# Optimization experiments

Measured on AMD Instinct MI355X. Metric: run time of the kernel, lower is better.

The kernel has to match this reference:

```python
import jax, jax.numpy as jnp
import numpy as np

K = 3  # kernel_size; padding = 1, stride = 1


def setup_inputs() -> dict:
    key = jax.random.key(0)
    ks = jax.random.split(key, 3)
    b, c, h, w = 8, 96, 256, 256
    x = jax.random.normal(ks[0], (b, c, h, w), dtype=jnp.float32)
    # attention MLP params: 1x1 convs on pooled vector == dense layers
    w1 = jax.random.normal(ks[1], (c // 8, c), dtype=jnp.float32) * (1.0 / np.sqrt(c))
    b1 = jnp.zeros((c // 8,), dtype=jnp.float32)
    w2 = jax.random.normal(ks[2], (K * K, c // 8), dtype=jnp.float32) * (1.0 / np.sqrt(c // 8))
    b2 = jnp.zeros((K * K,), dtype=jnp.float32)
    return {"x": x, "w1": w1, "b1": b1, "w2": w2, "b2": b2}


def reference(x, w1, b1, w2, b2):
    b, c, h, w = x.shape
    # attention: global avg pool -> 1x1 conv -> relu -> 1x1 conv -> softmax over k^2
    pooled = x.mean(axis=(2, 3))                       # (b, c)
    hid = jax.nn.relu(pooled @ w1.T + b1)              # (b, c//8)
    kw = jax.nn.softmax(hid @ w2.T + b2, axis=1)       # (b, k^2), per-batch kernel
    # dynamic depthwise conv: weighted sum of k^2 shifted views (no unfold materialization)
    xp = jnp.pad(x, ((0, 0), (0, 0), (1, 1), (1, 1)))
    out = jnp.zeros_like(x)
    for p in range(K * K):  # F.unfold ordering: row-major over kernel window
        di, dj = p // K, p % K
        out = out + kw[:, p, None, None, None] * xp[:, :, di:di + h, dj:dj + w]
    return out
```

## Files before the change

kernel.cpp:

```cpp
#include <hip/hip_runtime.h>
#include <math.h>


#define NB 8
#define NC 96
#define HH 256
#define WW 256
#define PLANE (HH * WW)
#define NPLANES (NB * NC)

__global__ __launch_bounds__(256) void pool_kernel(const float* __restrict__ x,
                                                   float* __restrict__ pooled) {
    const int plane = blockIdx.x;
    const int tid = threadIdx.x;
    const float4* xp = (const float4*)x + (size_t)plane * (PLANE / 4);
    float s = 0.f;
#pragma unroll 8
    for (int k = 0; k < 64; ++k) {
        float4 v = xp[k * 256 + tid];
        s += v.x + v.y + v.z + v.w;
    }
#pragma unroll
    for (int off = 32; off > 0; off >>= 1) s += __shfl_down(s, off);
    __shared__ float ws[4];
    if ((tid & 63) == 0) ws[tid >> 6] = s;
    __syncthreads();
    if (tid == 0)
        pooled[plane] = (ws[0] + ws[1] + ws[2] + ws[3]) * (1.0f / (float)PLANE);
}

__global__ __launch_bounds__(128) void attn_kernel(const float* __restrict__ pooled,
                                                   const float* __restrict__ w1,
                                                   const float* __restrict__ b1,
                                                   const float* __restrict__ w2,
                                                   const float* __restrict__ b2,
                                                   float* __restrict__ kw) {
    const int b = blockIdx.x;
    const int tid = threadIdx.x;
    __shared__ float p[NC];
    __shared__ float hid[12];
    __shared__ float logit[9];
    if (tid < NC) p[tid] = pooled[b * NC + tid];
    __syncthreads();
    if (tid < 12) {
        float a = b1[tid];
#pragma unroll
        for (int c = 0; c < NC; ++c) a = fmaf(p[c], w1[tid * NC + c], a);
        hid[tid] = a > 0.f ? a : 0.f;
    }
    __syncthreads();
    if (tid < 9) {
        float a = b2[tid];
#pragma unroll
        for (int j = 0; j < 12; ++j) a = fmaf(hid[j], w2[tid * 12 + j], a);
        logit[tid] = a;
    }
    __syncthreads();
    if (tid == 0) {
        float m = logit[0];
#pragma unroll
        for (int q = 1; q < 9; ++q) m = fmaxf(m, logit[q]);
        float e[9], s = 0.f;
#pragma unroll
        for (int q = 0; q < 9; ++q) { e[q] = __expf(logit[q] - m); s += e[q]; }
        float inv = 1.f / s;
#pragma unroll
        for (int q = 0; q < 9; ++q) kw[b * 9 + q] = e[q] * inv;
    }
}

__device__ __forceinline__ void accum_row(const float* __restrict__ row, int t,
                                          float w0, float w1, float w2, float4& o) {
    const int jc = t << 2;
    float4 cc = *(const float4*)(row + jc);
    float lm = (t > 0) ? row[jc - 1] : 0.f;
    float rp = (t < (WW / 4 - 1)) ? row[jc + 4] : 0.f;
    o.x = fmaf(w0, lm,   fmaf(w1, cc.x, fmaf(w2, cc.y, o.x)));
    o.y = fmaf(w0, cc.x, fmaf(w1, cc.y, fmaf(w2, cc.z, o.y)));
    o.z = fmaf(w0, cc.y, fmaf(w1, cc.z, fmaf(w2, cc.w, o.z)));
    o.w = fmaf(w0, cc.z, fmaf(w1, cc.w, fmaf(w2, rp,   o.w)));
}

__global__ __launch_bounds__(256) void conv_kernel(const float* __restrict__ x,
                                                   const float* __restrict__ kw9,
                                                   float* __restrict__ out) {
    const int q = blockIdx.x * 256 + threadIdx.x;
    const int i = q >> 6;
    const int t = q & 63;

    const size_t base = ((size_t)(blockIdx.z * NC + blockIdx.y)) * PLANE;
    const float* xpl = x + base;

    float w[9];
#pragma unroll
    for (int p = 0; p < 9; ++p) w[p] = kw9[blockIdx.z * 9 + p];

    float4 o = {0.f, 0.f, 0.f, 0.f};
    if (i > 0)        accum_row(xpl + (size_t)(i - 1) * WW, t, w[0], w[1], w[2], o);
                      accum_row(xpl + (size_t)i * WW,       t, w[3], w[4], w[5], o);
    if (i < HH - 1)   accum_row(xpl + (size_t)(i + 1) * WW, t, w[6], w[7], w[8], o);

    *(float4*)(out + base + (size_t)i * WW + (t << 2)) = o;
}

extern "C" void kernel_launch(void* const* d_in, const int* in_sizes, int n_in,
                              void* d_out, int out_size, void* d_ws, size_t ws_size,
                              hipStream_t stream) {
    const float* x  = (const float*)d_in[0];
    const float* w1 = (const float*)d_in[1];
    const float* b1 = (const float*)d_in[2];
    const float* w2 = (const float*)d_in[3];
    const float* b2 = (const float*)d_in[4];
    float* out = (float*)d_out;

    float* pooled = (float*)d_ws;
    float* kw     = pooled + NPLANES;

    pool_kernel<<<NPLANES, 256, 0, stream>>>(x, pooled);
    attn_kernel<<<NB, 128, 0, stream>>>(pooled, w1, b1, w2, b2, kw);
    dim3 grid(PLANE / (4 * 256), NC, NB);
    conv_kernel<<<grid, 256, 0, stream>>>(x, kw, out);
}
```

Before: 424.9 us.

## Stream rows per wavefront with register reuse, shuffled halos, and nontemporal stores

The conv kernel now gives each 64-lane wavefront a strip of 32 rows and slides a three-row register window down it. Each input row is loaded once instead of three times. Horizontal halo values come from wavefront shuffles instead of extra scalar global loads, and outputs use nontemporal stores. The grid shrinks to 2x96x8 blocks (1536 blocks of 256 threads, 6144 wavefronts), so there is less parallelism and a serial dependency along rows, which may limit latency hiding.

```diff
diff --git a/kernel.cpp b/kernel.cpp
--- a/kernel.cpp
+++ b/kernel.cpp
@@ -9,15 +9,17 @@
 #define PLANE (HH * WW)
 #define NPLANES (NB * NC)
 
+typedef float vfloat4 __attribute__((ext_vector_type(4)));
+
 __global__ __launch_bounds__(256) void pool_kernel(const float* __restrict__ x,
                                                    float* __restrict__ pooled) {
     const int plane = blockIdx.x;
     const int tid = threadIdx.x;
-    const float4* xp = (const float4*)x + (size_t)plane * (PLANE / 4);
+    const vfloat4* xp = (const vfloat4*)x + (size_t)plane * (PLANE / 4);
     float s = 0.f;
 #pragma unroll 8
     for (int k = 0; k < 64; ++k) {
-        float4 v = xp[k * 256 + tid];
+        vfloat4 v = xp[k * 256 + tid];
         s += v.x + v.y + v.z + v.w;
     }
 #pragma unroll
@@ -69,38 +71,62 @@
     }
 }
 
-__device__ __forceinline__ void accum_row(const float* __restrict__ row, int t,
-                                          float w0, float w1, float w2, float4& o) {
-    const int jc = t << 2;
-    float4 cc = *(const float4*)(row + jc);
-    float lm = (t > 0) ? row[jc - 1] : 0.f;
-    float rp = (t < (WW / 4 - 1)) ? row[jc + 4] : 0.f;
-    o.x = fmaf(w0, lm,   fmaf(w1, cc.x, fmaf(w2, cc.y, o.x)));
-    o.y = fmaf(w0, cc.x, fmaf(w1, cc.y, fmaf(w2, cc.z, o.y)));
-    o.z = fmaf(w0, cc.y, fmaf(w1, cc.z, fmaf(w2, cc.w, o.z)));
-    o.w = fmaf(w0, cc.z, fmaf(w1, cc.w, fmaf(w2, rp,   o.w)));
+struct Row {
+    vfloat4 v;
+    float hl, hr;
+};
+
+__device__ __forceinline__ Row load_row(const float* __restrict__ rowp, int lane) {
+    Row r;
+    r.v = *(const vfloat4*)(rowp + (lane << 2));
+    float up = __shfl_up(r.v.w, 1);
+    float dn = __shfl_down(r.v.x, 1);
+    r.hl = (lane == 0) ? 0.f : up;
+    r.hr = (lane == 63) ? 0.f : dn;
+    return r;
+}
+
+__device__ __forceinline__ Row zero_row() {
+    Row r; r.v = (vfloat4){0.f, 0.f, 0.f, 0.f}; r.hl = 0.f; r.hr = 0.f; return r;
+}
+
+__device__ __forceinline__ void row_fma(const Row& r, float wl, float wc, float wr,
+                                        vfloat4& o) {
+    o.x = fmaf(wl, r.hl,  fmaf(wc, r.v.x, fmaf(wr, r.v.y, o.x)));
+    o.y = fmaf(wl, r.v.x, fmaf(wc, r.v.y, fmaf(wr, r.v.z, o.y)));
+    o.z = fmaf(wl, r.v.y, fmaf(wc, r.v.z, fmaf(wr, r.v.w, o.z)));
+    o.w = fmaf(wl, r.v.z, fmaf(wc, r.v.w, fmaf(wr, r.hr,  o.w)));
 }
 
 __global__ __launch_bounds__(256) void conv_kernel(const float* __restrict__ x,
                                                    const float* __restrict__ kw9,
                                                    float* __restrict__ out) {
-    const int q = blockIdx.x * 256 + threadIdx.x;
-    const int i = q >> 6;
-    const int t = q & 63;
+    const int lane = threadIdx.x & 63;
+    const int strip = (blockIdx.x << 2) + (threadIdx.x >> 6);
+    const int rs = strip << 5;
 
     const size_t base = ((size_t)(blockIdx.z * NC + blockIdx.y)) * PLANE;
     const float* xpl = x + base;
+    float* opl = out + base;
 
     float w[9];
 #pragma unroll
     for (int p = 0; p < 9; ++p) w[p] = kw9[blockIdx.z * 9 + p];
 
-    float4 o = {0.f, 0.f, 0.f, 0.f};
-    if (i > 0)        accum_row(xpl + (size_t)(i - 1) * WW, t, w[0], w[1], w[2], o);
-                      accum_row(xpl + (size_t)i * WW,       t, w[3], w[4], w[5], o);
-    if (i < HH - 1)   accum_row(xpl + (size_t)(i + 1) * WW, t, w[6], w[7], w[8], o);
+    Row a = (rs == 0) ? zero_row() : load_row(xpl + (size_t)(rs - 1) * WW, lane);
+    Row b = load_row(xpl + (size_t)rs * WW, lane);
 
-    *(float4*)(out + base + (size_t)i * WW + (t << 2)) = o;
+#pragma unroll 4
+    for (int i = rs; i < rs + 32; ++i) {
+        Row c = (i + 1 < HH) ? load_row(xpl + (size_t)(i + 1) * WW, lane)
+                             : zero_row();
+        vfloat4 o = (vfloat4){0.f, 0.f, 0.f, 0.f};
+        row_fma(a, w[0], w[1], w[2], o);
+        row_fma(b, w[3], w[4], w[5], o);
+        row_fma(c, w[6], w[7], w[8], o);
+        __builtin_nontemporal_store(o, (vfloat4*)(opl + (size_t)i * WW + (lane << 2)));
+        a = b; b = c;
+    }
 }
 
 extern "C" void kernel_launch(void* const* d_in, const int* in_sizes, int n_in,
@@ -118,6 +144,6 @@
 
     pool_kernel<<<NPLANES, 256, 0, stream>>>(x, pooled);
     attn_kernel<<<NB, 128, 0, stream>>>(pooled, w1, b1, w2, b2, kw);
-    dim3 grid(PLANE / (4 * 256), NC, NB);
+    dim3 grid(2, NC, NB);
     conv_kernel<<<grid, 256, 0, stream>>>(x, kw, out);
 }
```

Measured after the change: 374.2 us. 11.9% less time.
